# Performance work log

Measured on AMD Instinct MI355X. Metric: run time of the kernel, lower is better.

Reference implementation:

```python
import jax, jax.numpy as jnp
import numpy as np

BATCH, DIM, HID, T = 1024, 1024, 4096, 16


def setup_inputs() -> dict:
    key = jax.random.key(0)
    k1, k2, k3 = jax.random.split(key, 3)
    # small init scale keeps the tanh-MLP dynamics stable over t in [0, 1]
    return {
        "y_init": jax.random.normal(k1, (BATCH, DIM), dtype=jnp.float32),
        "t_span": jnp.linspace(0.0, 1.0, T, dtype=jnp.float32),
        "W1": jax.random.normal(k2, (DIM, HID), dtype=jnp.float32) * 0.02,
        "b1": jnp.zeros((HID,), dtype=jnp.float32),
        "W2": jax.random.normal(k3, (HID, DIM), dtype=jnp.float32) * 0.02,
        "b2": jnp.zeros((DIM,), dtype=jnp.float32),
    }


def _vf(t, y, W1, b1, W2, b2):
    # vector field f(t, y): 2-layer tanh MLP, [B, D] -> [B, D]
    return jnp.tanh(y @ W1 + b1) @ W2 + b2


def _solve(y_init, t_span, W1, b1, W2, b2):
    # Fixed-grid RK4 solve over consecutive t_span points -> traj [T, B, D]
    def rk4(y, ts):
        t0, t1 = ts
        h = t1 - t0
        k1 = _vf(t0, y, W1, b1, W2, b2)
        k2 = _vf(t0 + h * 0.5, y + h * 0.5 * k1, W1, b1, W2, b2)
        k3 = _vf(t0 + h * 0.5, y + h * 0.5 * k2, W1, b1, W2, b2)
        k4 = _vf(t1, y + h * k3, W1, b1, W2, b2)
        y_next = y + (h / 6.0) * (k1 + 2.0 * k2 + 2.0 * k3 + k4)
        return y_next, y_next

    _, ys = jax.lax.scan(rk4, y_init, (t_span[:-1], t_span[1:]))
    return jnp.concatenate([y_init[None], ys], axis=0)


def reference(y_init, t_span, W1, b1, W2, b2):
    traj = _solve(y_init, t_span, W1, b1, W2, b2)
    return (t_span, traj)
```

## Files before the change

kernel.cpp:

```cpp
#include <hip/hip_runtime.h>
#include <hip/hip_bf16.h>
#include <stdint.h>

#define BATCH 1024
#define DIM   1024
#define HID   4096
#define TPTS  16

typedef __attribute__((ext_vector_type(8))) short  short8;
typedef __attribute__((ext_vector_type(4))) float  floatx4;

__device__ __forceinline__ unsigned short f32_to_bf16_bits(float f) {
    union { float f; unsigned u; } v; v.f = f;
    return (unsigned short)((v.u + 0x7fffu + ((v.u >> 16) & 1u)) >> 16);
}

__device__ __forceinline__ void store_bf16x4(unsigned short* p, floatx4 v) {
    union { unsigned short u[4]; uint2 q; } pk;
    pk.u[0] = f32_to_bf16_bits(v[0]);
    pk.u[1] = f32_to_bf16_bits(v[1]);
    pk.u[2] = f32_to_bf16_bits(v[2]);
    pk.u[3] = f32_to_bf16_bits(v[3]);
    *(uint2*)p = pk.q;
}

__device__ __forceinline__ float fast_tanh(float x) {
    float e = __expf(2.0f * x);
    return 1.0f - 2.0f / (e + 1.0f);
}

__device__ __forceinline__ void g2l16(const unsigned short* g, char* l) {
    __builtin_amdgcn_global_load_lds(
        (const __attribute__((address_space(1))) void*)g,
        (__attribute__((address_space(3))) void*)l, 16, 0, 0);
}

template<int MODE>
__global__ __launch_bounds__(256, 2)
void gemm_bt(const unsigned short* __restrict__ A,
             const unsigned short* __restrict__ Bt,
             const float* __restrict__ bias,
             void* __restrict__ Cout,
             int lda, int ldb, int ldc, int K, long long partStride)
{
    __shared__ __align__(16) char smem[24576];
    char* sA = smem;
    char* sB = smem + 8192;

    const int tid  = threadIdx.x;
    const int wave = tid >> 6;
    const int lane = tid & 63;
    const int wn = wave * 32;
    const int lr = lane & 15;
    const int q  = lane >> 4;

    const int rowBase = blockIdx.y * 64;
    const int colBase = blockIdx.x * 128;
    const long long koff = (long long)blockIdx.z * K;

    const unsigned short* gp[6];
    char* lp[6];
#pragma unroll
    for (int j = 0; j < 6; ++j) {
        const int p  = (j * 256 + tid) * 16;
        const int pa = (j < 2) ? p : (p - 8192);
        const int row = pa >> 7;
        const int ch  = (pa >> 4) & 7;
        const int sc  = ch ^ (row & 7);
        if (j < 2)
            gp[j] = A + (long long)(rowBase + row) * lda + koff + sc * 8;
        else
            gp[j] = Bt + (long long)(colBase + row) * ldb + koff + sc * 8;
        lp[j] = smem + p;
    }

    floatx4 acc[4][2];
#pragma unroll
    for (int mi = 0; mi < 4; ++mi)
#pragma unroll
        for (int ni = 0; ni < 2; ++ni) {
            floatx4 z4 = {0.f, 0.f, 0.f, 0.f};
            acc[mi][ni] = z4;
        }

    const int xr = lr & 7;
    int aOff[4], bOff[2];
#pragma unroll
    for (int i = 0; i < 4; ++i) aOff[i] = (i * 16 + lr) * 128;
#pragma unroll
    for (int i = 0; i < 2; ++i) bOff[i] = (wn + i * 16 + lr) * 128;
    const int swz0 = ((0 + q) ^ xr) * 16;
    const int swz1 = ((4 + q) ^ xr) * 16;

    const int KB = K >> 6;
    for (int kb = 0; kb < KB; ++kb) {
        if (kb) __syncthreads();
        const int kadv = kb * 64;
#pragma unroll
        for (int j = 0; j < 6; ++j)
            g2l16(gp[j] + kadv, lp[j]);
        __syncthreads();

        short8 af[4][2], bfr[2][2];
#pragma unroll
        for (int i = 0; i < 4; ++i) {
            af[i][0] = *(const short8*)(sA + aOff[i] + swz0);
            af[i][1] = *(const short8*)(sA + aOff[i] + swz1);
        }
#pragma unroll
        for (int i = 0; i < 2; ++i) {
            bfr[i][0] = *(const short8*)(sB + bOff[i] + swz0);
            bfr[i][1] = *(const short8*)(sB + bOff[i] + swz1);
        }
#pragma unroll
        for (int g = 0; g < 2; ++g)
#pragma unroll
            for (int mi = 0; mi < 4; ++mi)
#pragma unroll
                for (int ni = 0; ni < 2; ++ni)
                    acc[mi][ni] = __builtin_amdgcn_mfma_f32_16x16x32_bf16(
                        af[mi][g], bfr[ni][g], acc[mi][ni], 0, 0, 0);
    }

    if (MODE == 1) {
        __syncthreads();
        float bias2[2];
#pragma unroll
        for (int ni = 0; ni < 2; ++ni)
            bias2[ni] = bias[colBase + wn + ni * 16 + lr];
        unsigned short* sC = (unsigned short*)smem;
#pragma unroll
        for (int mi = 0; mi < 4; ++mi)
#pragma unroll
            for (int ni = 0; ni < 2; ++ni)
#pragma unroll
                for (int r = 0; r < 4; ++r) {
                    const int row = mi * 16 + q * 4 + r;
                    const int col = wn + ni * 16 + lr;
                    sC[row * 136 + col] =
                        f32_to_bf16_bits(fast_tanh(acc[mi][ni][r] + bias2[ni]));
                }
        __syncthreads();
        unsigned short* C = (unsigned short*)Cout;
#pragma unroll
        for (int it = 0; it < 4; ++it) {
            const int row = it * 16 + (tid >> 4);
            const int cc  = (tid & 15) * 8;
            *(uint4*)(C + (long long)(rowBase + row) * ldc + colBase + cc) =
                *(const uint4*)(sC + row * 136 + cc);
        }
    } else {
        float* C = (float*)Cout + (long long)blockIdx.z * partStride;
#pragma unroll
        for (int mi = 0; mi < 4; ++mi)
#pragma unroll
            for (int ni = 0; ni < 2; ++ni) {
                const int r0 = rowBase + mi * 16 + q * 4;
                const int c  = colBase + wn + ni * 16 + lr;
#pragma unroll
                for (int r = 0; r < 4; ++r)
                    C[(long long)(r0 + r) * ldc + c] = acc[mi][ni][r];
            }
    }
}

__global__ void combine(const float* __restrict__ parts,
                        const float* __restrict__ b2,
                        const float* __restrict__ ycur,
                        const float* __restrict__ tspan,
                        int step, int mode,
                        float* __restrict__ kacc,
                        unsigned short* __restrict__ ybf,
                        float* __restrict__ ynext)
{
    const int i = blockIdx.x * blockDim.x + threadIdx.x;
    const float h = tspan[step + 1] - tspan[step];
    const int NV = BATCH * DIM / 4;
    const floatx4* p = (const floatx4*)parts;
    floatx4 k = p[i] + p[i + NV] + p[i + 2 * NV] + p[i + 3 * NV];
    k = k + *(const floatx4*)(b2 + ((i * 4) & (DIM - 1)));
    floatx4 y = ((const floatx4*)ycur)[i];
    floatx4* ka = (floatx4*)kacc;
    if (mode == 1) {
        ka[i] = k;
        store_bf16x4(ybf + i * 4, y + (0.5f * h) * k);
    } else if (mode == 2) {
        ka[i] = ka[i] + 2.0f * k;
        store_bf16x4(ybf + i * 4, y + (0.5f * h) * k);
    } else if (mode == 3) {
        ka[i] = ka[i] + 2.0f * k;
        store_bf16x4(ybf + i * 4, y + h * k);
    } else {
        floatx4 yn = y + (h * (1.0f / 6.0f)) * (ka[i] + k);
        ((floatx4*)ynext)[i] = yn;
        store_bf16x4(ybf + i * 4, yn);
    }
}

__global__ void transpose_cast(const float* __restrict__ in,
                               unsigned short* __restrict__ out, int R, int C)
{
    __shared__ float tile[32][33];
    const int bx = blockIdx.x * 32;
    const int by = blockIdx.y * 32;
    const int tx = threadIdx.x, ty = threadIdx.y;
#pragma unroll
    for (int i = 0; i < 4; ++i)
        tile[ty + i * 8][tx] = in[(long long)(by + ty + i * 8) * C + bx + tx];
    __syncthreads();
#pragma unroll
    for (int i = 0; i < 4; ++i)
        out[(long long)(bx + ty + i * 8) * R + by + tx] =
            f32_to_bf16_bits(tile[tx][ty + i * 8]);
}

__global__ void init_kernel(const float* __restrict__ y0,
                            const float* __restrict__ tspan,
                            float* __restrict__ out,
                            unsigned short* __restrict__ ybf)
{
    const int i = blockIdx.x * blockDim.x + threadIdx.x;
    floatx4 v = ((const floatx4*)y0)[i];
    ((floatx4*)(out + TPTS))[i] = v;
    store_bf16x4(ybf + i * 4, v);
    if (blockIdx.x == 0 && threadIdx.x < TPTS) out[threadIdx.x] = tspan[threadIdx.x];
}

extern "C" void kernel_launch(void* const* d_in, const int* in_sizes, int n_in,
                              void* d_out, int out_size, void* d_ws, size_t ws_size,
                              hipStream_t stream)
{
    (void)in_sizes; (void)n_in; (void)out_size; (void)ws_size;
    const float* y0    = (const float*)d_in[0];
    const float* tspan = (const float*)d_in[1];
    const float* W1    = (const float*)d_in[2];
    const float* b1    = (const float*)d_in[3];
    const float* W2    = (const float*)d_in[4];
    const float* b2    = (const float*)d_in[5];
    float* out = (float*)d_out;

    char* ws = (char*)d_ws;
    unsigned short* W1T = (unsigned short*)(ws);
    unsigned short* W2T = (unsigned short*)(ws + (8ll << 20));
    unsigned short* Ybf = (unsigned short*)(ws + (16ll << 20));
    unsigned short* Hbf = (unsigned short*)(ws + (18ll << 20));
    float* parts = (float*)(ws + (26ll << 20));
    float* kacc  = (float*)(ws + (42ll << 20));

    dim3 tb(32, 8);
    transpose_cast<<<dim3(HID / 32, DIM / 32), tb, 0, stream>>>(W1, W1T, DIM, HID);
    transpose_cast<<<dim3(DIM / 32, HID / 32), tb, 0, stream>>>(W2, W2T, HID, DIM);
    init_kernel<<<BATCH * DIM / 1024, 256, 0, stream>>>(y0, tspan, out, Ybf);

    float* traj = out + TPTS;
    for (int t = 0; t < TPTS - 1; ++t) {
        const float* ycur = traj + (long long)t * BATCH * DIM;
        float* ynext = traj + (long long)(t + 1) * BATCH * DIM;
        for (int e = 0; e < 4; ++e) {
            gemm_bt<1><<<dim3(HID / 128, BATCH / 64, 1), 256, 0, stream>>>(
                Ybf, W1T, b1, (void*)Hbf, DIM, DIM, HID, DIM, 0LL);
            gemm_bt<0><<<dim3(DIM / 128, BATCH / 64, 4), 256, 0, stream>>>(
                Hbf, W2T, nullptr, (void*)parts, HID, HID, DIM, HID / 4,
                (long long)BATCH * DIM);
            combine<<<BATCH * DIM / 1024, 256, 0, stream>>>(
                parts, b2, ycur, tspan, t, e + 1, kacc, Ybf, ynext);
        }
    }
}
```

Baseline: 2.602 ms.

## Double-buffer LDS tiles and remap block indices for XCD-aware scheduling

Doubles shared memory to two 24KB stages so the next K-tile's global-to-LDS loads are issued before the current tile's MFMA work, leaving one barrier per iteration instead of two. Also remaps linear block IDs so consecutive blocks, which the hardware spreads round-robin across XCDs, land on nearby tiles, with the aim of improving L2 reuse per XCD. The hardcoded grid dimensions in the remap tie the kernel to the launch shape. Doubling LDS per block may reduce occupancy.

```diff
diff --git a/kernel.cpp b/kernel.cpp
--- a/kernel.cpp
+++ b/kernel.cpp
@@ -43,9 +43,7 @@
              void* __restrict__ Cout,
              int lda, int ldb, int ldc, int K, long long partStride)
 {
-    __shared__ __align__(16) char smem[24576];
-    char* sA = smem;
-    char* sB = smem + 8192;
+    __shared__ __align__(16) char smem[49152];
 
     const int tid  = threadIdx.x;
     const int wave = tid >> 6;
@@ -54,12 +52,26 @@
     const int lr = lane & 15;
     const int q  = lane >> 4;
 
-    const int rowBase = blockIdx.y * 64;
-    const int colBase = blockIdx.x * 128;
-    const long long koff = (long long)blockIdx.z * K;
+    int rowBase, colBase, zIdx;
+    if (MODE == 1) {
+        const int lin = (int)blockIdx.x + ((int)blockIdx.y << 5);
+        const int swz = ((lin & 7) << 6) | (lin >> 3);
+        colBase = (swz >> 4) << 7;
+        rowBase = (swz & 15) << 6;
+        zIdx = 0;
+    } else {
+        const int lin = (int)blockIdx.x +
+                        (((int)blockIdx.y + ((int)blockIdx.z << 4)) << 3);
+        const int swz = ((lin & 7) << 6) | (lin >> 3);
+        zIdx = swz >> 7;
+        const int s = swz & 127;
+        colBase = (s & 7) << 7;
+        rowBase = (s >> 3) << 6;
+    }
+    const long long koff = (long long)zIdx * K;
 
     const unsigned short* gp[6];
-    char* lp[6];
+    int lo[6];
 #pragma unroll
     for (int j = 0; j < 6; ++j) {
         const int p  = (j * 256 + tid) * 16;
@@ -71,7 +83,7 @@
             gp[j] = A + (long long)(rowBase + row) * lda + koff + sc * 8;
         else
             gp[j] = Bt + (long long)(colBase + row) * ldb + koff + sc * 8;
-        lp[j] = smem + p;
+        lo[j] = p;
     }
 
     floatx4 acc[4][2];
@@ -93,24 +105,34 @@
     const int swz1 = ((4 + q) ^ xr) * 16;
 
     const int KB = K >> 6;
+
+#pragma unroll
+    for (int j = 0; j < 6; ++j)
+        g2l16(gp[j], smem + lo[j]);
+    __syncthreads();
+
+    int cur = 0;
     for (int kb = 0; kb < KB; ++kb) {
-        if (kb) __syncthreads();
-        const int kadv = kb * 64;
-#pragma unroll
-        for (int j = 0; j < 6; ++j)
-            g2l16(gp[j] + kadv, lp[j]);
-        __syncthreads();
+        if (kb + 1 < KB) {
+            const int kadv = (kb + 1) * 64;
+            char* nb = smem + (cur ^ 1) * 24576;
+#pragma unroll
+            for (int j = 0; j < 6; ++j)
+                g2l16(gp[j] + kadv, nb + lo[j]);
+        }
+        const char* sAb = smem + cur * 24576;
+        const char* sBb = sAb + 8192;
 
         short8 af[4][2], bfr[2][2];
 #pragma unroll
         for (int i = 0; i < 4; ++i) {
-            af[i][0] = *(const short8*)(sA + aOff[i] + swz0);
-            af[i][1] = *(const short8*)(sA + aOff[i] + swz1);
+            af[i][0] = *(const short8*)(sAb + aOff[i] + swz0);
+            af[i][1] = *(const short8*)(sAb + aOff[i] + swz1);
         }
 #pragma unroll
         for (int i = 0; i < 2; ++i) {
-            bfr[i][0] = *(const short8*)(sB + bOff[i] + swz0);
-            bfr[i][1] = *(const short8*)(sB + bOff[i] + swz1);
+            bfr[i][0] = *(const short8*)(sBb + bOff[i] + swz0);
+            bfr[i][1] = *(const short8*)(sBb + bOff[i] + swz1);
         }
 #pragma unroll
         for (int g = 0; g < 2; ++g)
@@ -120,10 +142,12 @@
                 for (int ni = 0; ni < 2; ++ni)
                     acc[mi][ni] = __builtin_amdgcn_mfma_f32_16x16x32_bf16(
                         af[mi][g], bfr[ni][g], acc[mi][ni], 0, 0, 0);
+
+        __syncthreads();
+        cur ^= 1;
     }
 
     if (MODE == 1) {
-        __syncthreads();
         float bias2[2];
 #pragma unroll
         for (int ni = 0; ni < 2; ++ni)
@@ -150,7 +174,7 @@
                 *(const uint4*)(sC + row * 136 + cc);
         }
     } else {
-        float* C = (float*)Cout + (long long)blockIdx.z * partStride;
+        float* C = (float*)Cout + (long long)zIdx * partStride;
 #pragma unroll
         for (int mi = 0; mi < 4; ++mi)
 #pragma unroll
```

New measurement: 2.276 ms. 1.14x faster.
